# Kernel tuning notes

Hardware: AMD Instinct MI355X
Metric: run time of the kernel (lower is better)

## Reference

```python
import jax, jax.numpy as jnp
import numpy as np

N_NODES = 50000
N_EDGES = 800000
LEAKY_SLOPE = 0.01
DROPOUT_P = 0.5


def _graph_conv(src, dst, x, W, b):
    """DGL GraphConv with norm='both': D_out^{-1/2} A D_in^{-1/2} X W + b."""
    n = x.shape[0]
    ones = jnp.ones((src.shape[0],), dtype=x.dtype)
    deg_out = jax.ops.segment_sum(ones, src, num_segments=n)  # out-degree of src nodes
    deg_in = jax.ops.segment_sum(ones, dst, num_segments=n)   # in-degree of dst nodes
    norm_src = jax.lax.rsqrt(jnp.maximum(deg_out, 1.0))
    norm_dst = jax.lax.rsqrt(jnp.maximum(deg_in, 1.0))
    h = (x * norm_src[:, None]) @ W          # apply weight before aggregation
    agg = jax.ops.segment_sum(h[src], dst, num_segments=n)  # SpMM aggregate
    return agg * norm_dst[:, None] + b


def _dropout(x, key, p=DROPOUT_P):
    keep = jax.random.bernoulli(key, 1.0 - p, x.shape)
    return jnp.where(keep, x / (1.0 - p), jnp.zeros((), x.dtype))


def setup_inputs() -> dict:
    key = jax.random.key(0)
    ks = jax.random.split(key, 8)
    features = jax.random.normal(ks[0], (N_NODES, 128), dtype=jnp.float32)
    src = jax.random.randint(ks[1], (N_EDGES,), 0, N_NODES, dtype=jnp.int64)
    dst = jax.random.randint(ks[2], (N_EDGES,), 0, N_NODES, dtype=jnp.int64)
    s1 = 1.0 / np.sqrt(128.0)
    s3 = 1.0 / np.sqrt(128.0)
    W1 = jax.random.normal(ks[3], (128, 128), dtype=jnp.float32) * s1
    W2 = jax.random.normal(ks[4], (128, 128), dtype=jnp.float32) * s1
    W3 = jax.random.normal(ks[5], (128, 64), dtype=jnp.float32) * s3
    b1 = jnp.zeros((128,), dtype=jnp.float32)
    b2 = jnp.zeros((128,), dtype=jnp.float32)
    b3 = jnp.zeros((64,), dtype=jnp.float32)
    return {"features": features, "src": src, "dst": dst,
            "W1": W1, "b1": b1, "W2": W2, "b2": b2, "W3": W3, "b3": b3}


def reference(features, src, dst, W1, b1, W2, b2, W3, b3):
    dk = jax.random.split(jax.random.key(42), 3)
    h = jax.nn.leaky_relu(_graph_conv(src, dst, features, W1, b1), LEAKY_SLOPE)
    h = _dropout(h, dk[0])
    h = jax.nn.leaky_relu(_graph_conv(src, dst, h, W2, b2), LEAKY_SLOPE)
    h = _dropout(h, dk[1])
    h = jax.nn.leaky_relu(_graph_conv(src, dst, h, W3, b3), LEAKY_SLOPE)
    h = _dropout(h, dk[2])
    return h
```

## Files before the change

kernel.cpp:

```cpp
#include <hip/hip_runtime.h>
#include <hip/hip_fp16.h>
#include <stdint.h>

using half8 = __attribute__((ext_vector_type(8))) _Float16;
using f32x4 = __attribute__((ext_vector_type(4))) float;

#define SLOT_CAP 64
#define LDW 136
#define NBINS 50176
#define NB32 12544
#define NCHUNK 128

#define TFR(r) { x0 += x1; x1 = (x1 << r) | (x1 >> (32 - r)); x1 ^= x0; }

__host__ __device__ inline void threefry2x32(uint32_t k0, uint32_t k1,
                                             uint32_t c0, uint32_t c1,
                                             uint32_t& o0, uint32_t& o1) {
  uint32_t ks2 = k0 ^ k1 ^ 0x1BD11BDAu;
  uint32_t x0 = c0 + k0, x1 = c1 + k1;
  TFR(13) TFR(15) TFR(26) TFR(6)  x0 += k1;  x1 += ks2 + 1u;
  TFR(17) TFR(29) TFR(16) TFR(24) x0 += ks2; x1 += k0 + 2u;
  TFR(13) TFR(15) TFR(26) TFR(6)  x0 += k0;  x1 += k1 + 3u;
  TFR(17) TFR(29) TFR(16) TFR(24) x0 += k1;  x1 += ks2 + 4u;
  TFR(13) TFR(15) TFR(26) TFR(6)  x0 += ks2; x1 += k0 + 5u;
  o0 = x0; o1 = x1;
}

__device__ inline float tf_uniform(uint32_t k0, uint32_t k1, uint32_t i) {
  uint32_t o0, o1;
  threefry2x32(k0, k1, 0u, i, o0, o1);
  uint32_t bits = o0 ^ o1;
  return __uint_as_float((bits >> 9) | 0x3F800000u) - 1.0f;
}

__device__ inline uint16_t f2h(float f) {
  union { _Float16 h; uint16_t u; } c; c.h = (_Float16)f; return c.u;
}
__device__ inline uint32_t pack2h(float a, float b) {
  return (uint32_t)f2h(a) | ((uint32_t)f2h(b) << 16);
}
__device__ inline __half2 u2h2(uint32_t u) {
  union { uint32_t u; __half2 h; } c; c.u = u; return c.h;
}

__device__ inline void hacc(__half2* a, uint4 r) {
  a[0] = __hadd2(a[0], u2h2(r.x));
  a[1] = __hadd2(a[1], u2h2(r.y));
  a[2] = __hadd2(a[2], u2h2(r.z));
  a[3] = __hadd2(a[3], u2h2(r.w));
}

#define GDECL \
  uint4 A0, A1, A2, A3, A4, A5, A6, A7, B0, B1, B2, B3, B4, B5, B6, B7, \
        C0, C1, C2, C3, C4, C5, C6, C7, D0, D1, D2, D3, D4, D5, D6, D7;

#define GPTRS(sl, P) \
  const uint16_t* P##0 = hb + ((size_t)((sl).x & 0xFFFFu) << 7); \
  const uint16_t* P##1 = hb + ((size_t)((sl).x >> 16) << 7);     \
  const uint16_t* P##2 = hb + ((size_t)((sl).y & 0xFFFFu) << 7); \
  const uint16_t* P##3 = hb + ((size_t)((sl).y >> 16) << 7);     \
  const uint16_t* P##4 = hb + ((size_t)((sl).z & 0xFFFFu) << 7); \
  const uint16_t* P##5 = hb + ((size_t)((sl).z >> 16) << 7);     \
  const uint16_t* P##6 = hb + ((size_t)((sl).w & 0xFFFFu) << 7); \
  const uint16_t* P##7 = hb + ((size_t)((sl).w >> 16) << 7);

#define GLOAD(P, X, Y) \
  X##0 = *(const uint4*)P##0; Y##0 = *(const uint4*)(P##0 + 8); \
  X##1 = *(const uint4*)P##1; Y##1 = *(const uint4*)(P##1 + 8); \
  X##2 = *(const uint4*)P##2; Y##2 = *(const uint4*)(P##2 + 8); \
  X##3 = *(const uint4*)P##3; Y##3 = *(const uint4*)(P##3 + 8); \
  X##4 = *(const uint4*)P##4; Y##4 = *(const uint4*)(P##4 + 8); \
  X##5 = *(const uint4*)P##5; Y##5 = *(const uint4*)(P##5 + 8); \
  X##6 = *(const uint4*)P##6; Y##6 = *(const uint4*)(P##6 + 8); \
  X##7 = *(const uint4*)P##7; Y##7 = *(const uint4*)(P##7 + 8);

#define GHACC(X, Y) \
  hacc(ha, X##0); hacc(ha + 4, Y##0); \
  hacc(ha, X##1); hacc(ha + 4, Y##1); \
  hacc(ha, X##2); hacc(ha + 4, Y##2); \
  hacc(ha, X##3); hacc(ha + 4, Y##3); \
  hacc(ha, X##4); hacc(ha + 4, Y##4); \
  hacc(ha, X##5); hacc(ha + 4, Y##5); \
  hacc(ha, X##6); hacc(ha + 4, Y##6); \
  hacc(ha, X##7); hacc(ha + 4, Y##7);

#define ODECL uint4 A0, A1, A2, A3, A4, A5, A6, A7, C0, C1, C2, C3, C4, C5, C6, C7;

#define OPTRS(sl, P) \
  const uint16_t* P##0 = hb + ((size_t)((sl).x & 0xFFFFu) << 6); \
  const uint16_t* P##1 = hb + ((size_t)((sl).x >> 16) << 6);     \
  const uint16_t* P##2 = hb + ((size_t)((sl).y & 0xFFFFu) << 6); \
  const uint16_t* P##3 = hb + ((size_t)((sl).y >> 16) << 6);     \
  const uint16_t* P##4 = hb + ((size_t)((sl).z & 0xFFFFu) << 6); \
  const uint16_t* P##5 = hb + ((size_t)((sl).z >> 16) << 6);     \
  const uint16_t* P##6 = hb + ((size_t)((sl).w & 0xFFFFu) << 6); \
  const uint16_t* P##7 = hb + ((size_t)((sl).w >> 16) << 6);

#define OLOAD(P, X) \
  X##0 = *(const uint4*)P##0; X##1 = *(const uint4*)P##1; \
  X##2 = *(const uint4*)P##2; X##3 = *(const uint4*)P##3; \
  X##4 = *(const uint4*)P##4; X##5 = *(const uint4*)P##5; \
  X##6 = *(const uint4*)P##6; X##7 = *(const uint4*)P##7;

#define OHACC(X) \
  hacc(ha, X##0); hacc(ha, X##1); hacc(ha, X##2); hacc(ha, X##3); \
  hacc(ha, X##4); hacc(ha, X##5); hacc(ha, X##6); hacc(ha, X##7);

__global__ __launch_bounds__(256) void build_hist_kernel(
    const int* __restrict__ src, const int* __restrict__ dst,
    uint8_t* __restrict__ histD8, uint8_t* __restrict__ histS8,
    uint8_t* __restrict__ rank8,
    const float* __restrict__ W1, const float* __restrict__ W2,
    const float* __restrict__ W3, uint16_t* __restrict__ Wt,
    uint16_t* __restrict__ edge_slots,
    int n, int nE, int EPB) {
  const int bid = (int)blockIdx.x;
  if (bid >= 416) {
    const uint32_t pk = ((uint32_t)n << 16) | (uint32_t)(n & 0xFFFF);
    uint4 f; f.x = pk; f.y = pk; f.z = pk; f.w = pk;
    uint4* es4 = (uint4*)edge_slots;
    const int total = n * (SLOT_CAP / 8);
    for (int i = (bid - 416) * 256 + (int)threadIdx.x; i < total; i += 256 * 256)
      es4[i] = f;
    return;
  }
  if (bid >= 256) {
    int i = (bid - 256) * 256 + (int)threadIdx.x;
    float v;
    if (i < 16384) {
      int nr = i >> 7, k = i & 127;
      v = W1[k * 128 + nr];
    } else if (i < 32768) {
      int j = i - 16384, nr = j >> 7, k = j & 127;
      v = W2[k * 128 + nr];
    } else if (i < 40960) {
      int j = i - 32768, nr = j >> 7, k = j & 127;
      v = W3[k * 64 + nr];
    } else return;
    Wt[i] = f2h(v);
    return;
  }

  __shared__ uint32_t bins[NB32];
  const bool isSrc = bid >= 128;
  const int c = bid & 127;

  for (int i = threadIdx.x; i < NB32; i += 256) bins[i] = 0u;
  __syncthreads();

  const int e0 = c * EPB, e1 = min(e0 + EPB, nE);
  if (isSrc) {
    for (int e = e0 + (int)threadIdx.x; e < e1; e += 256) {
      const int k = src[e];
      atomicAdd(&bins[k >> 2], 1u << ((k & 3) * 8));
    }
  } else {
    for (int e = e0 + (int)threadIdx.x; e < e1; e += 256) {
      const int k = dst[e];
      const uint32_t old = atomicAdd(&bins[k >> 2], 1u << ((k & 3) * 8));
      rank8[e] = (uint8_t)((old >> ((k & 3) * 8)) & 0xFFu);
    }
  }
  __syncthreads();

  uint32_t* out = (uint32_t*)((isSrc ? histS8 : histD8) + (size_t)c * NBINS);
  for (int i = threadIdx.x; i < NB32; i += 256) out[i] = bins[i];
}

__global__ __launch_bounds__(256) void reduce_kernel(
    uint8_t* __restrict__ histD8, const uint8_t* __restrict__ histS8,
    int* __restrict__ degin, float* __restrict__ nsrc, int n) {
  const int v = ((int)blockIdx.x * 256 + (int)threadIdx.x) * 4;
  if (v >= n) return;

  uint32_t r0 = 0, r1 = 0, r2 = 0, r3 = 0;
  #pragma unroll 4
  for (int c = 0; c < NCHUNK; ++c) {
    uint32_t* p = (uint32_t*)(histD8 + (size_t)c * NBINS + v);
    const uint32_t w = *p;
    *p = min(r0, 255u) | (min(r1, 255u) << 8) |
         (min(r2, 255u) << 16) | (min(r3, 255u) << 24);
    r0 += w & 0xFFu; r1 += (w >> 8) & 0xFFu;
    r2 += (w >> 16) & 0xFFu; r3 += (w >> 24) & 0xFFu;
  }
  if (v + 3 < n) {
    *(int4*)&degin[v] = make_int4((int)r0, (int)r1, (int)r2, (int)r3);
  } else {
    const uint32_t rr[4] = {r0, r1, r2, r3};
    for (int j = 0; v + j < n; ++j) degin[v + j] = (int)rr[j];
  }

  uint32_t s0 = 0, s1 = 0, s2 = 0, s3 = 0;
  #pragma unroll 4
  for (int c = 0; c < NCHUNK; ++c) {
    const uint32_t w = *(const uint32_t*)(histS8 + (size_t)c * NBINS + v);
    s0 += w & 0xFFu; s1 += (w >> 8) & 0xFFu;
    s2 += (w >> 16) & 0xFFu; s3 += (w >> 24) & 0xFFu;
  }
  if (v + 3 < n) {
    float4 f;
    f.x = rsqrtf(fmaxf((float)s0, 1.0f));
    f.y = rsqrtf(fmaxf((float)s1, 1.0f));
    f.z = rsqrtf(fmaxf((float)s2, 1.0f));
    f.w = rsqrtf(fmaxf((float)s3, 1.0f));
    *(float4*)&nsrc[v] = f;
  } else {
    const uint32_t ss[4] = {s0, s1, s2, s3};
    for (int j = 0; v + j < n; ++j)
      nsrc[v + j] = rsqrtf(fmaxf((float)ss[j], 1.0f));
  }
}

__global__ __launch_bounds__(256) void scatter_gemm1_kernel(
    const int* __restrict__ src, const int* __restrict__ dst,
    const uint8_t* __restrict__ cum8, const uint8_t* __restrict__ rank8,
    uint16_t* __restrict__ edge_slots,
    const float* __restrict__ X, const float* __restrict__ nsrc,
    const uint16_t* __restrict__ Wt1, uint16_t* __restrict__ h1,
    int n, int nE, int EPB) {
  const int bid = (int)blockIdx.x;

  if (bid < NCHUNK) {
    const int c = bid;
    const uint8_t* cum = cum8 + (size_t)c * NBINS;
    const int e0 = c * EPB, e1 = min(e0 + EPB, nE);
    for (int e = e0 + (int)threadIdx.x; e < e1; e += 256) {
      const int d = dst[e];
      const int pos = (int)cum[d] + (int)rank8[e];
      if (pos < SLOT_CAP) edge_slots[((size_t)d << 6) + pos] = (uint16_t)src[e];
    }
    return;
  }

  const int r0 = (bid - NCHUNK) * 64;
  const int tid = (int)threadIdx.x;
  const int wave = tid >> 6, lane = tid & 63;
  const int wm = wave & 1, wn = wave >> 1;
  const int lane15 = lane & 15, quad = lane >> 4;

  const int rowA0 = r0 + wm * 32 + lane15;
  const int rowA1 = rowA0 + 16;
  const bool v0 = rowA0 < n, v1 = rowA1 < n;

  f32x4 acc[2][4] = {};
  #pragma unroll
  for (int kc = 0; kc < 128; kc += 32) {
    const int ko = kc + quad * 8;
    half8 a0 = {}, a1 = {};
    if (v0) {
      float4 x0 = *(const float4*)&X[(size_t)rowA0 * 128 + ko];
      float4 x1 = *(const float4*)&X[(size_t)rowA0 * 128 + ko + 4];
      a0[0] = (_Float16)x0.x; a0[1] = (_Float16)x0.y;
      a0[2] = (_Float16)x0.z; a0[3] = (_Float16)x0.w;
      a0[4] = (_Float16)x1.x; a0[5] = (_Float16)x1.y;
      a0[6] = (_Float16)x1.z; a0[7] = (_Float16)x1.w;
    }
    if (v1) {
      float4 x0 = *(const float4*)&X[(size_t)rowA1 * 128 + ko];
      float4 x1 = *(const float4*)&X[(size_t)rowA1 * 128 + ko + 4];
      a1[0] = (_Float16)x0.x; a1[1] = (_Float16)x0.y;
      a1[2] = (_Float16)x0.z; a1[3] = (_Float16)x0.w;
      a1[4] = (_Float16)x1.x; a1[5] = (_Float16)x1.y;
      a1[6] = (_Float16)x1.z; a1[7] = (_Float16)x1.w;
    }
    #pragma unroll
    for (int nt = 0; nt < 4; ++nt) {
      int nn = wn * 64 + nt * 16 + lane15;
      half8 b = *(const half8*)&Wt1[nn * 128 + ko];
      acc[0][nt] = __builtin_amdgcn_mfma_f32_16x16x32_f16(a0, b, acc[0][nt], 0, 0, 0);
      acc[1][nt] = __builtin_amdgcn_mfma_f32_16x16x32_f16(a1, b, acc[1][nt], 0, 0, 0);
    }
  }

  #pragma unroll
  for (int mt = 0; mt < 2; ++mt) {
    #pragma unroll
    for (int reg = 0; reg < 4; ++reg) {
      int row = r0 + wm * 32 + mt * 16 + quad * 4 + reg;
      float nsr = (row < n) ? nsrc[row] : 0.0f;
      #pragma unroll
      for (int nt = 0; nt < 4; ++nt) {
        int col = wn * 64 + nt * 16 + lane15;
        h1[(size_t)row * 128 + col] = f2h(acc[mt][nt][reg] * nsr);
      }
    }
  }
}

template<int NCOLS>
__global__ __launch_bounds__(256, 3) void fuse_gather_gemm_kernel(
    const uint16_t* __restrict__ h_in, const int* __restrict__ degin,
    const uint16_t* __restrict__ edge_slots, const float* __restrict__ nsrc,
    const float* __restrict__ bias, const uint16_t* __restrict__ Wt,
    uint16_t* __restrict__ h_out, uint32_t k0, uint32_t k1, int n) {
  __shared__ uint16_t Xs[32 * LDW];
  __shared__ float ns_s[32];
  const int r0 = (int)blockIdx.x * 32;
  const int tid = (int)threadIdx.x;

  if (tid < 32) {
    int row = r0 + tid;
    ns_s[tid] = (row < n) ? nsrc[row] : 1.0f;
  }

  const int nl = tid >> 3;
  const int node = r0 + nl;
  const int c16 = (tid & 7) * 16;

  if (node < n) {
    __half2 ha[8];
    #pragma unroll
    for (int j = 0; j < 8; ++j) ha[j] = __half2(__float2half(0.f), __float2half(0.f));

    const int dgi = degin[node];
    const int deg = min(dgi, SLOT_CAP);
    const uint16_t* slots = edge_slots + ((size_t)node << 6);
    const uint16_t* hb = h_in + c16;
    const int nb = (deg + 7) >> 3;

    GDECL
    if (nb > 0) {
      uint4 sA = *(const uint4*)&slots[0];
      GPTRS(sA, p)
      GLOAD(p, A, B)
      int b = 1;
      for (; b + 1 < nb; b += 2) {
        uint4 sB = *(const uint4*)&slots[b * 8];
        uint4 sC = *(const uint4*)&slots[b * 8 + 8];
        GPTRS(sB, q)
        GLOAD(q, C, D)
        GHACC(A, B)
        GPTRS(sC, r)
        GLOAD(r, A, B)
        GHACC(C, D)
      }
      if (b < nb) {
        uint4 sB = *(const uint4*)&slots[b * 8];
        GPTRS(sB, q)
        GLOAD(q, C, D)
        GHACC(A, B)
        GHACC(C, D)
      } else {
        GHACC(A, B)
      }
    }

    float acc[16];
    #pragma unroll
    for (int j = 0; j < 8; ++j) {
      float2 f = __half22float2(ha[j]);
      acc[2 * j] = f.x; acc[2 * j + 1] = f.y;
    }

    const float nd = rsqrtf(fmaxf((float)dgi, 1.0f));
    const float4 b0 = *(const float4*)&bias[c16];
    const float4 b1 = *(const float4*)&bias[c16 + 4];
    const float4 b2 = *(const float4*)&bias[c16 + 8];
    const float4 b3 = *(const float4*)&bias[c16 + 12];
    const float bb[16] = {b0.x, b0.y, b0.z, b0.w, b1.x, b1.y, b1.z, b1.w,
                          b2.x, b2.y, b2.z, b2.w, b3.x, b3.y, b3.z, b3.w};
    const uint32_t i0 = (uint32_t)(node * 128 + c16);

    float o[16];
    #pragma unroll
    for (int j = 0; j < 16; ++j) {
      float v = acc[j] * nd + bb[j];
      v = (v >= 0.f) ? v : 0.01f * v;
      o[j] = (tf_uniform(k0, k1, i0 + (uint32_t)j) < 0.5f) ? v * 2.0f : 0.0f;
    }

    uint4 w0, w1;
    w0.x = pack2h(o[0], o[1]);   w0.y = pack2h(o[2], o[3]);
    w0.z = pack2h(o[4], o[5]);   w0.w = pack2h(o[6], o[7]);
    w1.x = pack2h(o[8], o[9]);   w1.y = pack2h(o[10], o[11]);
    w1.z = pack2h(o[12], o[13]); w1.w = pack2h(o[14], o[15]);
    *(uint4*)&Xs[nl * LDW + c16] = w0;
    *(uint4*)&Xs[nl * LDW + c16 + 8] = w1;
  } else {
    uint4 z = make_uint4(0u, 0u, 0u, 0u);
    *(uint4*)&Xs[nl * LDW + c16] = z;
    *(uint4*)&Xs[nl * LDW + c16 + 8] = z;
  }
  __syncthreads();

  const int wave = tid >> 6, lane = tid & 63;
  const int wm = wave & 1, wn = wave >> 1;
  const int lane15 = lane & 15, quad = lane >> 4;
  constexpr int NT = NCOLS / 32;

  f32x4 acc[NT] = {};
  #pragma unroll
  for (int kc = 0; kc < 128; kc += 32) {
    const int ko = kc + quad * 8;
    half8 a = *(const half8*)&Xs[(wm * 16 + lane15) * LDW + ko];
    #pragma unroll
    for (int nt = 0; nt < NT; ++nt) {
      int nn = wn * (NCOLS / 2) + nt * 16 + lane15;
      half8 b = *(const half8*)&Wt[nn * 128 + ko];
      acc[nt] = __builtin_amdgcn_mfma_f32_16x16x32_f16(a, b, acc[nt], 0, 0, 0);
    }
  }

  #pragma unroll
  for (int nt = 0; nt < NT; ++nt) {
    #pragma unroll
    for (int reg = 0; reg < 4; ++reg) {
      int rl = wm * 16 + quad * 4 + reg;
      int row = r0 + rl;
      int col = wn * (NCOLS / 2) + nt * 16 + lane15;
      h_out[(size_t)row * NCOLS + col] = f2h(acc[nt][reg] * ns_s[rl]);
    }
  }
}

__global__ __launch_bounds__(256, 4) void gather_out_kernel(
    const uint16_t* __restrict__ h3, const int* __restrict__ degin,
    const uint16_t* __restrict__ edge_slots, const float* __restrict__ bias,
    float* __restrict__ out, uint32_t k0, uint32_t k1, int n) {
  const int node = (int)blockIdx.x * 32 + (int)(threadIdx.x >> 3);
  if (node >= n) return;
  const int c8 = (threadIdx.x & 7) * 8;

  const int dgi = degin[node];
  const int deg = min(dgi, SLOT_CAP);
  const uint16_t* slots = edge_slots + ((size_t)node << 6);
  const uint16_t* hb = h3 + c8;
  const int nb = (deg + 7) >> 3;

  __half2 ha[4];
  #pragma unroll
  for (int j = 0; j < 4; ++j) ha[j] = __half2(__float2half(0.f), __float2half(0.f));

  ODECL
  if (nb > 0) {
    uint4 sA = *(const uint4*)&slots[0];
    OPTRS(sA, p)
    OLOAD(p, A)
    int b = 1;
    for (; b + 1 < nb; b += 2) {
      uint4 sB = *(const uint4*)&slots[b * 8];
      uint4 sC = *(const uint4*)&slots[b * 8 + 8];
      OPTRS(sB, q)
      OLOAD(q, C)
      OHACC(A)
      OPTRS(sC, r)
      OLOAD(r, A)
      OHACC(C)
    }
    if (b < nb) {
      uint4 sB = *(const uint4*)&slots[b * 8];
      OPTRS(sB, q)
      OLOAD(q, C)
      OHACC(A)
      OHACC(C)
    } else {
      OHACC(A)
    }
  }

  float acc[8];
  #pragma unroll
  for (int j = 0; j < 4; ++j) {
    float2 f = __half22float2(ha[j]);
    acc[2 * j] = f.x; acc[2 * j + 1] = f.y;
  }

  const float nd = rsqrtf(fmaxf((float)dgi, 1.0f));
  const float4 b0 = *(const float4*)&bias[c8];
  const float4 b1 = *(const float4*)&bias[c8 + 4];
  const float bb[8] = {b0.x, b0.y, b0.z, b0.w, b1.x, b1.y, b1.z, b1.w};
  const uint32_t i0 = (uint32_t)(node * 64 + c8);

  float o[8];
  #pragma unroll
  for (int j = 0; j < 8; ++j) {
    float v = acc[j] * nd + bb[j];
    v = (v >= 0.f) ? v : 0.01f * v;
    o[j] = (tf_uniform(k0, k1, i0 + (uint32_t)j) < 0.5f) ? v * 2.0f : 0.0f;
  }

  float* op = &out[(size_t)node * 64 + c8];
  *(float4*)op = make_float4(o[0], o[1], o[2], o[3]);
  *(float4*)(op + 4) = make_float4(o[4], o[5], o[6], o[7]);
}

extern "C" void kernel_launch(void* const* d_in, const int* in_sizes, int n_in,
                              void* d_out, int out_size, void* d_ws, size_t ws_size,
                              hipStream_t stream) {
  const float* features = (const float*)d_in[0];
  const int*   src      = (const int*)d_in[1];
  const int*   dst      = (const int*)d_in[2];
  const float* W1       = (const float*)d_in[3];
  const float* b1       = (const float*)d_in[4];
  const float* W2       = (const float*)d_in[5];
  const float* b2       = (const float*)d_in[6];
  const float* W3       = (const float*)d_in[7];
  const float* b3       = (const float*)d_in[8];
  float* out = (float*)d_out;

  const int n  = in_sizes[0] / 128;
  const int nE = in_sizes[1];
  const int nA = ((n + 63) / 64) * 64;

  char* p = (char*)d_ws;
  uint8_t* histD8      = (uint8_t*)p;  p += (size_t)NCHUNK * NBINS;
  uint8_t* histS8      = (uint8_t*)p;  p += (size_t)NCHUNK * NBINS;
  uint8_t* rank8       = (uint8_t*)p;  p += ((size_t)nE + 3) & ~(size_t)3;
  int* degin           = (int*)p;      p += (size_t)n * 4;
  float* nsrc          = (float*)p;    p += (size_t)n * 4;
  uint16_t* edge_slots = (uint16_t*)p; p += (size_t)n * SLOT_CAP * 2;
  uint16_t* Wt         = (uint16_t*)p; p += 40960 * 2;
  uint16_t* h1         = (uint16_t*)p; p += (size_t)nA * 128 * 2;
  uint16_t* h2         = (uint16_t*)p; p += (size_t)nA * 128 * 2;
  uint16_t* h3         = (uint16_t*)p;

  uint32_t dk[3][2];
  for (uint32_t i = 0; i < 3; ++i)
    threefry2x32(0u, 42u, 0u, i, dk[i][0], dk[i][1]);

  const int EPB = (nE + NCHUNK - 1) / NCHUNK;
  const int gb64 = (n + 63) / 64;
  const int gb32 = (n + 31) / 32;

  build_hist_kernel<<<672, 256, 0, stream>>>(src, dst, histD8, histS8, rank8,
                                             W1, W2, W3, Wt, edge_slots,
                                             n, nE, EPB);
  reduce_kernel<<<((n + 3) / 4 + 255) / 256, 256, 0, stream>>>(
      histD8, histS8, degin, nsrc, n);
  scatter_gemm1_kernel<<<NCHUNK + gb64, 256, 0, stream>>>(
      src, dst, histD8, rank8, edge_slots, features, nsrc, Wt, h1, n, nE, EPB);
  fuse_gather_gemm_kernel<128><<<gb32, 256, 0, stream>>>(
      h1, degin, edge_slots, nsrc, b1, Wt + 16384, h2, dk[0][0], dk[0][1], n);
  fuse_gather_gemm_kernel<64><<<gb32, 256, 0, stream>>>(
      h2, degin, edge_slots, nsrc, b2, Wt + 32768, h3, dk[1][0], dk[1][1], n);
  gather_out_kernel<<<gb32, 256, 0, stream>>>(
      h3, degin, edge_slots, b3, out, dk[2][0], dk[2][1], n);
}
```

Measured before the change: 248.7 us.

## Fuse reduce, scatter, GEMM and gather layers into persistent megakernel with grid barriers

Replaces the reduce, scatter+GEMM1, two fused gather-GEMM launches and the output gather with one persistent kernel of 768 blocks. The phases are separated by a software grid barrier: an atomic counter with acquire/release ordering and sleep-spinning, reset by the histogram kernel. The goal is to remove per-launch overhead and the tail effects between the dependent stages. The cost is that all blocks must be co-resident or the barrier deadlocks. Work is also redistributed: the first GEMM now uses 32-row tiles and the edge scatter is spread across the whole grid. Spin-wait barriers add latency of their own.

```diff
diff --git a/kernel.cpp b/kernel.cpp
--- a/kernel.cpp
+++ b/kernel.cpp
@@ -10,6 +10,7 @@
 #define NBINS 50176
 #define NB32 12544
 #define NCHUNK 128
+#define MGRID 768
 
 #define TFR(r) { x0 += x1; x1 = (x1 << r) | (x1 >> (32 - r)); x1 ^= x0; }
 
@@ -50,6 +51,17 @@
   a[3] = __hadd2(a[3], u2h2(r.w));
 }
 
+__device__ inline void gsync(int* cnt, int target) {
+  __syncthreads();
+  if (threadIdx.x == 0) {
+    __hip_atomic_fetch_add(cnt, 1, __ATOMIC_ACQ_REL, __HIP_MEMORY_SCOPE_AGENT);
+    while (__hip_atomic_load(cnt, __ATOMIC_ACQUIRE,
+                             __HIP_MEMORY_SCOPE_AGENT) < target)
+      __builtin_amdgcn_s_sleep(2);
+  }
+  __syncthreads();
+}
+
 #define GDECL \
   uint4 A0, A1, A2, A3, A4, A5, A6, A7, B0, B1, B2, B3, B4, B5, B6, B7, \
         C0, C1, C2, C3, C4, C5, C6, C7, D0, D1, D2, D3, D4, D5, D6, D7;
@@ -112,9 +124,10 @@
     uint8_t* __restrict__ rank8,
     const float* __restrict__ W1, const float* __restrict__ W2,
     const float* __restrict__ W3, uint16_t* __restrict__ Wt,
-    uint16_t* __restrict__ edge_slots,
+    uint16_t* __restrict__ edge_slots, int* __restrict__ sync_cnt,
     int n, int nE, int EPB) {
   const int bid = (int)blockIdx.x;
+  if (bid == 0 && threadIdx.x == 0) *sync_cnt = 0;
   if (bid >= 416) {
     const uint32_t pk = ((uint32_t)n << 16) | (uint32_t)(n & 0xFFFF);
     uint4 f; f.x = pk; f.y = pk; f.z = pk; f.w = pk;
@@ -167,136 +180,15 @@
   for (int i = threadIdx.x; i < NB32; i += 256) out[i] = bins[i];
 }
 
-__global__ __launch_bounds__(256) void reduce_kernel(
-    uint8_t* __restrict__ histD8, const uint8_t* __restrict__ histS8,
-    int* __restrict__ degin, float* __restrict__ nsrc, int n) {
-  const int v = ((int)blockIdx.x * 256 + (int)threadIdx.x) * 4;
-  if (v >= n) return;
-
-  uint32_t r0 = 0, r1 = 0, r2 = 0, r3 = 0;
-  #pragma unroll 4
-  for (int c = 0; c < NCHUNK; ++c) {
-    uint32_t* p = (uint32_t*)(histD8 + (size_t)c * NBINS + v);
-    const uint32_t w = *p;
-    *p = min(r0, 255u) | (min(r1, 255u) << 8) |
-         (min(r2, 255u) << 16) | (min(r3, 255u) << 24);
-    r0 += w & 0xFFu; r1 += (w >> 8) & 0xFFu;
-    r2 += (w >> 16) & 0xFFu; r3 += (w >> 24) & 0xFFu;
-  }
-  if (v + 3 < n) {
-    *(int4*)&degin[v] = make_int4((int)r0, (int)r1, (int)r2, (int)r3);
-  } else {
-    const uint32_t rr[4] = {r0, r1, r2, r3};
-    for (int j = 0; v + j < n; ++j) degin[v + j] = (int)rr[j];
-  }
-
-  uint32_t s0 = 0, s1 = 0, s2 = 0, s3 = 0;
-  #pragma unroll 4
-  for (int c = 0; c < NCHUNK; ++c) {
-    const uint32_t w = *(const uint32_t*)(histS8 + (size_t)c * NBINS + v);
-    s0 += w & 0xFFu; s1 += (w >> 8) & 0xFFu;
-    s2 += (w >> 16) & 0xFFu; s3 += (w >> 24) & 0xFFu;
-  }
-  if (v + 3 < n) {
-    float4 f;
-    f.x = rsqrtf(fmaxf((float)s0, 1.0f));
-    f.y = rsqrtf(fmaxf((float)s1, 1.0f));
-    f.z = rsqrtf(fmaxf((float)s2, 1.0f));
-    f.w = rsqrtf(fmaxf((float)s3, 1.0f));
-    *(float4*)&nsrc[v] = f;
-  } else {
-    const uint32_t ss[4] = {s0, s1, s2, s3};
-    for (int j = 0; v + j < n; ++j)
-      nsrc[v + j] = rsqrtf(fmaxf((float)ss[j], 1.0f));
-  }
-}
-
-__global__ __launch_bounds__(256) void scatter_gemm1_kernel(
-    const int* __restrict__ src, const int* __restrict__ dst,
-    const uint8_t* __restrict__ cum8, const uint8_t* __restrict__ rank8,
-    uint16_t* __restrict__ edge_slots,
-    const float* __restrict__ X, const float* __restrict__ nsrc,
-    const uint16_t* __restrict__ Wt1, uint16_t* __restrict__ h1,
-    int n, int nE, int EPB) {
-  const int bid = (int)blockIdx.x;
-
-  if (bid < NCHUNK) {
-    const int c = bid;
-    const uint8_t* cum = cum8 + (size_t)c * NBINS;
-    const int e0 = c * EPB, e1 = min(e0 + EPB, nE);
-    for (int e = e0 + (int)threadIdx.x; e < e1; e += 256) {
-      const int d = dst[e];
-      const int pos = (int)cum[d] + (int)rank8[e];
-      if (pos < SLOT_CAP) edge_slots[((size_t)d << 6) + pos] = (uint16_t)src[e];
-    }
-    return;
-  }
-
-  const int r0 = (bid - NCHUNK) * 64;
-  const int tid = (int)threadIdx.x;
-  const int wave = tid >> 6, lane = tid & 63;
-  const int wm = wave & 1, wn = wave >> 1;
-  const int lane15 = lane & 15, quad = lane >> 4;
-
-  const int rowA0 = r0 + wm * 32 + lane15;
-  const int rowA1 = rowA0 + 16;
-  const bool v0 = rowA0 < n, v1 = rowA1 < n;
-
-  f32x4 acc[2][4] = {};
-  #pragma unroll
-  for (int kc = 0; kc < 128; kc += 32) {
-    const int ko = kc + quad * 8;
-    half8 a0 = {}, a1 = {};
-    if (v0) {
-      float4 x0 = *(const float4*)&X[(size_t)rowA0 * 128 + ko];
-      float4 x1 = *(const float4*)&X[(size_t)rowA0 * 128 + ko + 4];
-      a0[0] = (_Float16)x0.x; a0[1] = (_Float16)x0.y;
-      a0[2] = (_Float16)x0.z; a0[3] = (_Float16)x0.w;
-      a0[4] = (_Float16)x1.x; a0[5] = (_Float16)x1.y;
-      a0[6] = (_Float16)x1.z; a0[7] = (_Float16)x1.w;
-    }
-    if (v1) {
-      float4 x0 = *(const float4*)&X[(size_t)rowA1 * 128 + ko];
-      float4 x1 = *(const float4*)&X[(size_t)rowA1 * 128 + ko + 4];
-      a1[0] = (_Float16)x0.x; a1[1] = (_Float16)x0.y;
-      a1[2] = (_Float16)x0.z; a1[3] = (_Float16)x0.w;
-      a1[4] = (_Float16)x1.x; a1[5] = (_Float16)x1.y;
-      a1[6] = (_Float16)x1.z; a1[7] = (_Float16)x1.w;
-    }
-    #pragma unroll
-    for (int nt = 0; nt < 4; ++nt) {
-      int nn = wn * 64 + nt * 16 + lane15;
-      half8 b = *(const half8*)&Wt1[nn * 128 + ko];
-      acc[0][nt] = __builtin_amdgcn_mfma_f32_16x16x32_f16(a0, b, acc[0][nt], 0, 0, 0);
-      acc[1][nt] = __builtin_amdgcn_mfma_f32_16x16x32_f16(a1, b, acc[1][nt], 0, 0, 0);
-    }
-  }
-
-  #pragma unroll
-  for (int mt = 0; mt < 2; ++mt) {
-    #pragma unroll
-    for (int reg = 0; reg < 4; ++reg) {
-      int row = r0 + wm * 32 + mt * 16 + quad * 4 + reg;
-      float nsr = (row < n) ? nsrc[row] : 0.0f;
-      #pragma unroll
-      for (int nt = 0; nt < 4; ++nt) {
-        int col = wn * 64 + nt * 16 + lane15;
-        h1[(size_t)row * 128 + col] = f2h(acc[mt][nt][reg] * nsr);
-      }
-    }
-  }
-}
-
 template<int NCOLS>
-__global__ __launch_bounds__(256, 3) void fuse_gather_gemm_kernel(
-    const uint16_t* __restrict__ h_in, const int* __restrict__ degin,
+__device__ inline void fuse_tile(
+    int t, const uint16_t* __restrict__ h_in, const int* __restrict__ degin,
     const uint16_t* __restrict__ edge_slots, const float* __restrict__ nsrc,
     const float* __restrict__ bias, const uint16_t* __restrict__ Wt,
-    uint16_t* __restrict__ h_out, uint32_t k0, uint32_t k1, int n) {
-  __shared__ uint16_t Xs[32 * LDW];
-  __shared__ float ns_s[32];
-  const int r0 = (int)blockIdx.x * 32;
-  const int tid = (int)threadIdx.x;
+    uint16_t* __restrict__ h_out, uint32_t k0, uint32_t k1, int n,
+    int tid, uint16_t* Xs, float* ns_s) {
+  __syncthreads();
+  const int r0 = t * 32;
 
   if (tid < 32) {
     int row = r0 + tid;
@@ -413,75 +305,191 @@
   }
 }
 
-__global__ __launch_bounds__(256, 4) void gather_out_kernel(
-    const uint16_t* __restrict__ h3, const int* __restrict__ degin,
-    const uint16_t* __restrict__ edge_slots, const float* __restrict__ bias,
-    float* __restrict__ out, uint32_t k0, uint32_t k1, int n) {
-  const int node = (int)blockIdx.x * 32 + (int)(threadIdx.x >> 3);
-  if (node >= n) return;
-  const int c8 = (threadIdx.x & 7) * 8;
-
-  const int dgi = degin[node];
-  const int deg = min(dgi, SLOT_CAP);
-  const uint16_t* slots = edge_slots + ((size_t)node << 6);
-  const uint16_t* hb = h3 + c8;
-  const int nb = (deg + 7) >> 3;
-
-  __half2 ha[4];
-  #pragma unroll
-  for (int j = 0; j < 4; ++j) ha[j] = __half2(__float2half(0.f), __float2half(0.f));
-
-  ODECL
-  if (nb > 0) {
-    uint4 sA = *(const uint4*)&slots[0];
-    OPTRS(sA, p)
-    OLOAD(p, A)
-    int b = 1;
-    for (; b + 1 < nb; b += 2) {
-      uint4 sB = *(const uint4*)&slots[b * 8];
-      uint4 sC = *(const uint4*)&slots[b * 8 + 8];
-      OPTRS(sB, q)
-      OLOAD(q, C)
-      OHACC(A)
-      OPTRS(sC, r)
-      OLOAD(r, A)
-      OHACC(C)
-    }
-    if (b < nb) {
-      uint4 sB = *(const uint4*)&slots[b * 8];
-      OPTRS(sB, q)
-      OLOAD(q, C)
-      OHACC(A)
-      OHACC(C)
-    } else {
-      OHACC(A)
-    }
-  }
-
-  float acc[8];
-  #pragma unroll
-  for (int j = 0; j < 4; ++j) {
-    float2 f = __half22float2(ha[j]);
-    acc[2 * j] = f.x; acc[2 * j + 1] = f.y;
-  }
-
-  const float nd = rsqrtf(fmaxf((float)dgi, 1.0f));
-  const float4 b0 = *(const float4*)&bias[c8];
-  const float4 b1 = *(const float4*)&bias[c8 + 4];
-  const float bb[8] = {b0.x, b0.y, b0.z, b0.w, b1.x, b1.y, b1.z, b1.w};
-  const uint32_t i0 = (uint32_t)(node * 64 + c8);
-
-  float o[8];
-  #pragma unroll
-  for (int j = 0; j < 8; ++j) {
-    float v = acc[j] * nd + bb[j];
-    v = (v >= 0.f) ? v : 0.01f * v;
-    o[j] = (tf_uniform(k0, k1, i0 + (uint32_t)j) < 0.5f) ? v * 2.0f : 0.0f;
-  }
-
-  float* op = &out[(size_t)node * 64 + c8];
-  *(float4*)op = make_float4(o[0], o[1], o[2], o[3]);
-  *(float4*)(op + 4) = make_float4(o[4], o[5], o[6], o[7]);
+__global__ __launch_bounds__(256, 3) void mega_kernel(
+    const int* __restrict__ src, const int* __restrict__ dst,
+    uint8_t* __restrict__ histD8, const uint8_t* __restrict__ histS8,
+    const uint8_t* __restrict__ rank8, uint16_t* __restrict__ edge_slots,
+    int* __restrict__ degin, float* __restrict__ nsrc,
+    const float* __restrict__ X, const uint16_t* __restrict__ Wt,
+    const float* __restrict__ b1, const float* __restrict__ b2,
+    const float* __restrict__ b3,
+    uint16_t* __restrict__ h1, uint16_t* __restrict__ h2,
+    uint16_t* __restrict__ h3, float* __restrict__ out,
+    uint32_t k00, uint32_t k01, uint32_t k10, uint32_t k11,
+    uint32_t k20, uint32_t k21,
+    int n, int nE, int EPB, int ntiles, int* __restrict__ cnt) {
+  __shared__ uint16_t Xs[32 * LDW];
+  __shared__ float ns_s[32];
+  const int bid = (int)blockIdx.x;
+  const int tid = (int)threadIdx.x;
+
+  {
+    const int v = (bid * 256 + tid) * 4;
+    if (v < n) {
+      uint32_t r0 = 0, r1 = 0, r2 = 0, r3 = 0;
+      #pragma unroll 4
+      for (int c = 0; c < NCHUNK; ++c) {
+        uint32_t* p = (uint32_t*)(histD8 + (size_t)c * NBINS + v);
+        const uint32_t w = *p;
+        *p = min(r0, 255u) | (min(r1, 255u) << 8) |
+             (min(r2, 255u) << 16) | (min(r3, 255u) << 24);
+        r0 += w & 0xFFu; r1 += (w >> 8) & 0xFFu;
+        r2 += (w >> 16) & 0xFFu; r3 += (w >> 24) & 0xFFu;
+      }
+      if (v + 3 < n) {
+        *(int4*)&degin[v] = make_int4((int)r0, (int)r1, (int)r2, (int)r3);
+      } else {
+        const uint32_t rr[4] = {r0, r1, r2, r3};
+        for (int j = 0; v + j < n; ++j) degin[v + j] = (int)rr[j];
+      }
+      uint32_t s0 = 0, s1 = 0, s2 = 0, s3 = 0;
+      #pragma unroll 4
+      for (int c = 0; c < NCHUNK; ++c) {
+        const uint32_t w = *(const uint32_t*)(histS8 + (size_t)c * NBINS + v);
+        s0 += w & 0xFFu; s1 += (w >> 8) & 0xFFu;
+        s2 += (w >> 16) & 0xFFu; s3 += (w >> 24) & 0xFFu;
+      }
+      if (v + 3 < n) {
+        float4 f;
+        f.x = rsqrtf(fmaxf((float)s0, 1.0f));
+        f.y = rsqrtf(fmaxf((float)s1, 1.0f));
+        f.z = rsqrtf(fmaxf((float)s2, 1.0f));
+        f.w = rsqrtf(fmaxf((float)s3, 1.0f));
+        *(float4*)&nsrc[v] = f;
+      } else {
+        const uint32_t ss[4] = {s0, s1, s2, s3};
+        for (int j = 0; v + j < n; ++j)
+          nsrc[v + j] = rsqrtf(fmaxf((float)ss[j], 1.0f));
+      }
+    }
+  }
+  gsync(cnt, MGRID);
+
+  for (int e = bid * 256 + tid; e < nE; e += MGRID * 256) {
+    const int c = e / EPB;
+    const int d = dst[e];
+    const int pos = (int)histD8[(size_t)c * NBINS + d] + (int)rank8[e];
+    if (pos < SLOT_CAP) edge_slots[((size_t)d << 6) + pos] = (uint16_t)src[e];
+  }
+  {
+    const int wave = tid >> 6, lane = tid & 63;
+    const int wm = wave & 1, wn = wave >> 1;
+    const int lane15 = lane & 15, quad = lane >> 4;
+    for (int t = bid; t < ntiles; t += MGRID) {
+      const int r0 = t * 32;
+      const int rowA = r0 + wm * 16 + lane15;
+      const bool va = rowA < n;
+      f32x4 acc[4] = {};
+      #pragma unroll
+      for (int kc = 0; kc < 128; kc += 32) {
+        const int ko = kc + quad * 8;
+        half8 a = {};
+        if (va) {
+          float4 x0 = *(const float4*)&X[(size_t)rowA * 128 + ko];
+          float4 x1 = *(const float4*)&X[(size_t)rowA * 128 + ko + 4];
+          a[0] = (_Float16)x0.x; a[1] = (_Float16)x0.y;
+          a[2] = (_Float16)x0.z; a[3] = (_Float16)x0.w;
+          a[4] = (_Float16)x1.x; a[5] = (_Float16)x1.y;
+          a[6] = (_Float16)x1.z; a[7] = (_Float16)x1.w;
+        }
+        #pragma unroll
+        for (int nt = 0; nt < 4; ++nt) {
+          int nn = wn * 64 + nt * 16 + lane15;
+          half8 b = *(const half8*)&Wt[nn * 128 + ko];
+          acc[nt] = __builtin_amdgcn_mfma_f32_16x16x32_f16(a, b, acc[nt], 0, 0, 0);
+        }
+      }
+      #pragma unroll
+      for (int reg = 0; reg < 4; ++reg) {
+        const int row = r0 + wm * 16 + quad * 4 + reg;
+        const float nsr = (row < n) ? nsrc[row] : 0.0f;
+        #pragma unroll
+        for (int nt = 0; nt < 4; ++nt) {
+          int col = wn * 64 + nt * 16 + lane15;
+          h1[(size_t)row * 128 + col] = f2h(acc[nt][reg] * nsr);
+        }
+      }
+    }
+  }
+  gsync(cnt, 2 * MGRID);
+
+  for (int t = bid; t < ntiles; t += MGRID)
+    fuse_tile<128>(t, h1, degin, edge_slots, nsrc, b1, Wt + 16384, h2,
+                   k00, k01, n, tid, Xs, ns_s);
+  gsync(cnt, 3 * MGRID);
+
+  for (int t = bid; t < ntiles; t += MGRID)
+    fuse_tile<64>(t, h2, degin, edge_slots, nsrc, b2, Wt + 32768, h3,
+                  k10, k11, n, tid, Xs, ns_s);
+  gsync(cnt, 4 * MGRID);
+
+  for (int t = bid; t < ntiles; t += MGRID) {
+    const int node = t * 32 + (tid >> 3);
+    if (node >= n) continue;
+    const int c8 = (tid & 7) * 8;
+
+    const int dgi = degin[node];
+    const int deg = min(dgi, SLOT_CAP);
+    const uint16_t* slots = edge_slots + ((size_t)node << 6);
+    const uint16_t* hb = h3 + c8;
+    const int nb = (deg + 7) >> 3;
+
+    __half2 ha[4];
+    #pragma unroll
+    for (int j = 0; j < 4; ++j) ha[j] = __half2(__float2half(0.f), __float2half(0.f));
+
+    ODECL
+    if (nb > 0) {
+      uint4 sA = *(const uint4*)&slots[0];
+      OPTRS(sA, p)
+      OLOAD(p, A)
+      int b = 1;
+      for (; b + 1 < nb; b += 2) {
+        uint4 sB = *(const uint4*)&slots[b * 8];
+        uint4 sC = *(const uint4*)&slots[b * 8 + 8];
+        OPTRS(sB, q)
+        OLOAD(q, C)
+        OHACC(A)
+        OPTRS(sC, r)
+        OLOAD(r, A)
+        OHACC(C)
+      }
+      if (b < nb) {
+        uint4 sB = *(const uint4*)&slots[b * 8];
+        OPTRS(sB, q)
+        OLOAD(q, C)
+        OHACC(A)
+        OHACC(C)
+      } else {
+        OHACC(A)
+      }
+    }
+
+    float acc[8];
+    #pragma unroll
+    for (int j = 0; j < 4; ++j) {
+      float2 f = __half22float2(ha[j]);
+      acc[2 * j] = f.x; acc[2 * j + 1] = f.y;
+    }
+
+    const float nd = rsqrtf(fmaxf((float)dgi, 1.0f));
+    const float4 bb0 = *(const float4*)&b3[c8];
+    const float4 bb1 = *(const float4*)&b3[c8 + 4];
+    const float bb[8] = {bb0.x, bb0.y, bb0.z, bb0.w, bb1.x, bb1.y, bb1.z, bb1.w};
+    const uint32_t i0 = (uint32_t)(node * 64 + c8);
+
+    float o[8];
+    #pragma unroll
+    for (int j = 0; j < 8; ++j) {
+      float v = acc[j] * nd + bb[j];
+      v = (v >= 0.f) ? v : 0.01f * v;
+      o[j] = (tf_uniform(k20, k21, i0 + (uint32_t)j) < 0.5f) ? v * 2.0f : 0.0f;
+    }
+
+    float* op = &out[(size_t)node * 64 + c8];
+    *(float4*)op = make_float4(o[0], o[1], o[2], o[3]);
+    *(float4*)(op + 4) = make_float4(o[4], o[5], o[6], o[7]);
+  }
 }
 
 extern "C" void kernel_launch(void* const* d_in, const int* in_sizes, int n_in,
@@ -503,6 +511,7 @@
   const int nA = ((n + 63) / 64) * 64;
 
   char* p = (char*)d_ws;
+  int* sync_cnt        = (int*)p;      p += 256;
   uint8_t* histD8      = (uint8_t*)p;  p += (size_t)NCHUNK * NBINS;
   uint8_t* histS8      = (uint8_t*)p;  p += (size_t)NCHUNK * NBINS;
   uint8_t* rank8       = (uint8_t*)p;  p += ((size_t)nE + 3) & ~(size_t)3;
@@ -519,20 +528,14 @@
     threefry2x32(0u, 42u, 0u, i, dk[i][0], dk[i][1]);
 
   const int EPB = (nE + NCHUNK - 1) / NCHUNK;
-  const int gb64 = (n + 63) / 64;
-  const int gb32 = (n + 31) / 32;
+  const int ntiles = (n + 31) / 32;
 
   build_hist_kernel<<<672, 256, 0, stream>>>(src, dst, histD8, histS8, rank8,
                                              W1, W2, W3, Wt, edge_slots,
-                                             n, nE, EPB);
-  reduce_kernel<<<((n + 3) / 4 + 255) / 256, 256, 0, stream>>>(
-      histD8, histS8, degin, nsrc, n);
-  scatter_gemm1_kernel<<<NCHUNK + gb64, 256, 0, stream>>>(
-      src, dst, histD8, rank8, edge_slots, features, nsrc, Wt, h1, n, nE, EPB);
-  fuse_gather_gemm_kernel<128><<<gb32, 256, 0, stream>>>(
-      h1, degin, edge_slots, nsrc, b1, Wt + 16384, h2, dk[0][0], dk[0][1], n);
-  fuse_gather_gemm_kernel<64><<<gb32, 256, 0, stream>>>(
-      h2, degin, edge_slots, nsrc, b2, Wt + 32768, h3, dk[1][0], dk[1][1], n);
-  gather_out_kernel<<<gb32, 256, 0, stream>>>(
-      h3, degin, edge_slots, b3, out, dk[2][0], dk[2][1], n);
-}
+                                             sync_cnt, n, nE, EPB);
+  mega_kernel<<<MGRID, 256, 0, stream>>>(
+      src, dst, histD8, histS8, rank8, edge_slots, degin, nsrc,
+      features, Wt, b1, b2, b3, h1, h2, h3, out,
+      dk[0][0], dk[0][1], dk[1][0], dk[1][1], dk[2][0], dk[2][1],
+      n, nE, EPB, ntiles, sync_cnt);
+}
```

After: 858.7 us. 3.45x slower.
